# Kernel tuning notes

Measured on AMD Instinct MI355X. Metric: run time of the kernel, lower is better.

Reference implementation:

```python
import jax, jax.numpy as jnp
import numpy as np

NUM_EXPERTS = 16
HIDDEN_DIM = 1024
TOP_K = 4
INPUT_DIM = 4096
OUTPUT_DIM = 4096
BATCH = 4096


def setup_inputs() -> dict:
    key = jax.random.key(0)
    ks = jax.random.split(key, 6)
    total_cols = NUM_EXPERTS * HIDDEN_DIM
    return {
        "x": jax.random.normal(ks[0], (BATCH, INPUT_DIM), dtype=jnp.float32),
        "gate_w": jax.random.normal(ks[1], (INPUT_DIM, NUM_EXPERTS), dtype=jnp.float32) * 0.02,
        "gate_b": jnp.zeros((NUM_EXPERTS,), dtype=jnp.float32),
        "weight": jax.random.normal(ks[2], (INPUT_DIM, total_cols), dtype=jnp.float32) * 0.01,
        "agg_w": jax.random.normal(ks[3], (total_cols, OUTPUT_DIM), dtype=jnp.float32) * 0.02,
        "agg_b": jnp.zeros((OUTPUT_DIM,), dtype=jnp.float32),
    }


def reference(x, gate_w, gate_b, weight, agg_w, agg_b):
    # 1) gating logits (batch, E), 2) sum over batch -> (E,)
    gating_logits = x @ gate_w + gate_b
    gating_sum = gating_logits.sum(axis=0)
    # 3) global top-k expert selection -> binary mask over experts
    _, topk_inds = jax.lax.top_k(gating_sum, TOP_K)
    expert_mask = jnp.zeros((NUM_EXPERTS,), dtype=x.dtype).at[topk_inds].set(1.0)
    # 4/5) block-sparse matmul: mask replicated over all row blocks, so each
    # expert's column block [e*H:(e+1)*H] is x @ W_block if selected else 0.
    out_sparse = x @ weight  # (batch, E*H)
    col_mask = jnp.repeat(expert_mask, HIDDEN_DIM)  # (E*H,)
    out_sparse = out_sparse * col_mask[None, :]
    # 6) aggregator
    final_out = out_sparse @ agg_w + agg_b
    return final_out
```

## Files before the change

kernel.cpp:

```cpp
#include <hip/hip_runtime.h>
#include <hip/hip_bf16.h>


#define BATCH 4096
#define DIN 4096
#define NE 16
#define HD 1024
#define TOPK 4
#define TOTC (NE * HD)
#define NT 64

using bf16 = __hip_bfloat16;
typedef __attribute__((ext_vector_type(8))) short short8;
typedef __attribute__((ext_vector_type(4))) float f32x4;

__device__ inline short f2bs(float f) {
  __hip_bfloat16 h = __float2bfloat16(f);
  return *reinterpret_cast<short*>(&h);
}

__global__ void k_cvtsum(const float* __restrict__ x, bf16* __restrict__ xb,
                         float* __restrict__ colsum) {
  const int t = threadIdx.x;
  const int lane = t & 63;
  const int w = t >> 6;
  const int c = blockIdx.x * 256 + lane * 4;
  const int r0 = blockIdx.y * 128 + w * 32;
  float4 s = {0.f, 0.f, 0.f, 0.f};
  for (int i = 0; i < 32; ++i) {
    size_t off = (size_t)(r0 + i) * DIN + c;
    float4 v = *reinterpret_cast<const float4*>(x + off);
    s.x += v.x; s.y += v.y; s.z += v.z; s.w += v.w;
    ushort4 b;
    b.x = (unsigned short)f2bs(v.x); b.y = (unsigned short)f2bs(v.y);
    b.z = (unsigned short)f2bs(v.z); b.w = (unsigned short)f2bs(v.w);
    *reinterpret_cast<ushort4*>(reinterpret_cast<char*>(xb) + off * 2) = b;
  }
  __shared__ float sm[4][256];
  sm[w][lane * 4 + 0] = s.x; sm[w][lane * 4 + 1] = s.y;
  sm[w][lane * 4 + 2] = s.z; sm[w][lane * 4 + 3] = s.w;
  __syncthreads();
  float tot = sm[0][t] + sm[1][t] + sm[2][t] + sm[3][t];
  atomicAdd(&colsum[blockIdx.x * 256 + t], tot);
}

__global__ void k_gate(const float* __restrict__ colsum, const float* __restrict__ gw,
                       const float* __restrict__ gb, int* __restrict__ ids) {
  __shared__ float red[4][16];
  __shared__ float gs[16];
  int t = threadIdx.x;
  int e = t & 15, kg = t >> 4;
  float p = 0.f;
  for (int k = kg; k < DIN; k += 16) p += colsum[k] * gw[(size_t)k * NE + e];
  p += __shfl_down(p, 32);
  p += __shfl_down(p, 16);
  if ((t & 63) < 16) red[t >> 6][e] = p;
  __syncthreads();
  if (t < 16) gs[t] = red[0][t] + red[1][t] + red[2][t] + red[3][t] + (float)BATCH * gb[t];
  __syncthreads();
  if (t == 0) {
    float v[16];
    #pragma unroll
    for (int i = 0; i < 16; ++i) v[i] = gs[i];
    for (int j = 0; j < TOPK; ++j) {
      int bi = 0;
      float bv = v[0];
      for (int i2 = 1; i2 < 16; ++i2)
        if (v[i2] > bv) { bv = v[i2]; bi = i2; }
      ids[j] = bi;
      v[bi] = -3.4e38f;
    }
  }
}

__global__ void k_gather_w(const float* __restrict__ w, const int* __restrict__ ids,
                           bf16* __restrict__ wbt) {
  __shared__ float tile[64 * 65];
  const int t = threadIdx.x;
  const int tc = t & 15, kr = t >> 4;
  const int tk = t & 7, nr = t >> 3;
  for (int tl = blockIdx.x; tl < 4096; tl += 1024) {
    const int k0 = (tl & 63) * 64, n0 = (tl >> 6) * 64;
    const int e = ids[n0 >> 10];
    const int wc0 = e * HD + (n0 & 1023);
    #pragma unroll
    for (int j = 0; j < 2; ++j) {
      int kk = kr + j * 32;
      float4 v = *reinterpret_cast<const float4*>(w + (size_t)(k0 + kk) * TOTC + wc0 + tc * 4);
      float* dst = &tile[kk * 65 + tc * 4];
      dst[0] = v.x; dst[1] = v.y; dst[2] = v.z; dst[3] = v.w;
    }
    __syncthreads();
    short8 r;
    #pragma unroll
    for (int m = 0; m < 8; ++m) r[m] = f2bs(tile[(tk * 8 + m) * 65 + nr]);
    *reinterpret_cast<short8*>(wbt + (size_t)(n0 + nr) * DIN + k0 + tk * 8) = r;
    __syncthreads();
  }
}

__global__ void k_gather_a(const float* __restrict__ a, const int* __restrict__ ids,
                           bf16* __restrict__ abt) {
  __shared__ float tile[64 * 65];
  const int t = threadIdx.x;
  const int tc = t & 15, kr = t >> 4;
  const int tk = t & 7, nr = t >> 3;
  for (int tl = blockIdx.x; tl < 4096; tl += 1024) {
    const int k0 = (tl & 63) * 64, n0 = (tl >> 6) * 64;
    const int e = ids[k0 >> 10];
    const int ar0 = e * HD + (k0 & 1023);
    #pragma unroll
    for (int j = 0; j < 2; ++j) {
      int kk = kr + j * 32;
      float4 v = *reinterpret_cast<const float4*>(a + (size_t)(ar0 + kk) * 4096 + n0 + tc * 4);
      float* dst = &tile[kk * 65 + tc * 4];
      dst[0] = v.x; dst[1] = v.y; dst[2] = v.z; dst[3] = v.w;
    }
    __syncthreads();
    short8 r;
    #pragma unroll
    for (int m = 0; m < 8; ++m) r[m] = f2bs(tile[(tk * 8 + m) * 65 + nr]);
    *reinterpret_cast<short8*>(abt + (size_t)(n0 + nr) * DIN + k0 + tk * 8) = r;
    __syncthreads();
  }
}

#define MFMA_BF16 __builtin_amdgcn_mfma_f32_16x16x32_bf16
#define VM4 asm volatile("s_waitcnt vmcnt(4)" ::: "memory")
#define VM0 asm volatile("s_waitcnt vmcnt(0)" ::: "memory")
#define NOST ((void)0)

#define PH(BUF, Q, STG, GATE)                                                   \
  do {                                                                          \
    if ((Q) == 0) {                                                             \
      _Pragma("unroll") for (int nf = 0; nf < 4; ++nf) {                        \
        bfrag[nf][0] = LDB(BUF, nf, 0);                                         \
        bfrag[nf][1] = LDB(BUF, nf, 1);                                         \
      }                                                                         \
    }                                                                           \
    short8 aA0 = LDA(BUF, 2 * (Q), 0), aA1 = LDA(BUF, 2 * (Q), 1);              \
    short8 aB0 = LDA(BUF, 2 * (Q) + 1, 0), aB1 = LDA(BUF, 2 * (Q) + 1, 1);      \
    STG;                                                                        \
    GATE;                                                                       \
    __builtin_amdgcn_sched_barrier(0);                                          \
    __builtin_amdgcn_s_barrier();                                               \
    asm volatile("s_waitcnt lgkmcnt(0)" ::: "memory");                          \
    __builtin_amdgcn_sched_barrier(0);                                          \
    __builtin_amdgcn_s_setprio(1);                                              \
    _Pragma("unroll") for (int nf = 0; nf < 4; ++nf) {                          \
      acc[2 * (Q)][nf] = MFMA_BF16(aA0, bfrag[nf][0], acc[2 * (Q)][nf], 0, 0, 0);       \
      acc[2 * (Q)][nf] = MFMA_BF16(aA1, bfrag[nf][1], acc[2 * (Q)][nf], 0, 0, 0);       \
      acc[2 * (Q) + 1][nf] = MFMA_BF16(aB0, bfrag[nf][0], acc[2 * (Q) + 1][nf], 0, 0, 0); \
      acc[2 * (Q) + 1][nf] = MFMA_BF16(aB1, bfrag[nf][1], acc[2 * (Q) + 1][nf], 0, 0, 0); \
    }                                                                           \
    __builtin_amdgcn_s_setprio(0);                                              \
    __builtin_amdgcn_s_barrier();                                               \
  } while (0)

template <int STORE_F32>
__global__ __launch_bounds__(512, 2) void k_gemm8(
    const bf16* __restrict__ A, const bf16* __restrict__ Bt,
    bf16* __restrict__ Cb, float* __restrict__ Cf, const float* __restrict__ bias) {
  __shared__ __align__(16) char smraw[131072];
  const int t = threadIdx.x;
  const int lane = t & 63;
  const int w = t >> 6;
  const int wr = w >> 2;
  const int wc = w & 3;

  const int bid = blockIdx.x;
  const int xcd = bid & 7;
  const int i = bid >> 3;
  const int bm = ((xcd >> 1) * 4 + (i & 3)) * 256;
  const int bn = ((xcd & 1) * 8 + (i >> 2)) * 256;

  f32x4 acc[8][4] = {};
  short8 bfrag[4][2];

  const int srow = w * 16 + (lane >> 3);
  const int sgr = lane & 7;

  auto STAGE_A = [&](int buf, int half, int kt) {
    char* lb = smraw + buf * 65536 + half * 16384 + w * 2048 + lane * 16;
    #pragma unroll
    for (int i2 = 0; i2 < 2; ++i2) {
      int r = srow + i2 * 8;
      const bf16* g = A + (size_t)(bm + half * 128 + r) * 4096 + kt * 64 + ((sgr ^ (r & 7)) * 8);
      __builtin_amdgcn_global_load_lds(
          (const __attribute__((address_space(1))) void*)g,
          (__attribute__((address_space(3))) void*)(lb + i2 * 1024), 16, 0, 0);
    }
  };
  auto STAGE_B = [&](int buf, int half, int kt) {
    char* lb = smraw + buf * 65536 + 32768 + half * 16384 + w * 2048 + lane * 16;
    #pragma unroll
    for (int i2 = 0; i2 < 2; ++i2) {
      int r = srow + i2 * 8;
      const bf16* g = Bt + (size_t)(bn + half * 128 + r) * 4096 + kt * 64 + ((sgr ^ (r & 7)) * 8);
      __builtin_amdgcn_global_load_lds(
          (const __attribute__((address_space(1))) void*)g,
          (__attribute__((address_space(3))) void*)(lb + i2 * 1024), 16, 0, 0);
    }
  };
  auto LDA = [&](int buf, int mf, int kk) -> short8 {
    int r = mf * 16 + (lane & 15);
    int kb = ((kk * 4 + (lane >> 4)) ^ (r & 7)) * 16;
    return *reinterpret_cast<const short8*>(smraw + buf * 65536 + wr * 16384 + r * 128 + kb);
  };
  auto LDB = [&](int buf, int nf, int kk) -> short8 {
    int nc = wc * 64 + nf * 16 + (lane & 15);
    int half = nc >> 7, r = nc & 127;
    int kb = ((kk * 4 + (lane >> 4)) ^ (r & 7)) * 16;
    return *reinterpret_cast<const short8*>(smraw + buf * 65536 + 32768 + half * 16384 + r * 128 + kb);
  };

  STAGE_B(0, 0, 0); STAGE_B(0, 1, 0);
  STAGE_A(0, 0, 0); STAGE_A(0, 1, 0);
  STAGE_B(1, 0, 1); STAGE_B(1, 1, 1);
  VM4;
  __builtin_amdgcn_s_barrier();

  for (int tt = 0; tt < 31; ++tt) {
    const int a = 2 * tt;
    PH(0, 0, STAGE_A(1, 0, a + 1), NOST);
    PH(0, 1, STAGE_A(1, 1, a + 1), NOST);
    PH(0, 2, STAGE_B(0, 0, a + 2), NOST);
    PH(0, 3, STAGE_B(0, 1, a + 2), VM4);
    PH(1, 0, STAGE_A(0, 0, a + 2), NOST);
    PH(1, 1, STAGE_A(0, 1, a + 2), NOST);
    PH(1, 2, STAGE_B(1, 0, a + 3), NOST);
    PH(1, 3, STAGE_B(1, 1, a + 3), VM4);
  }
  PH(0, 0, STAGE_A(1, 0, 63), NOST);
  PH(0, 1, STAGE_A(1, 1, 63), NOST);
  PH(0, 2, NOST, NOST);
  PH(0, 3, NOST, VM0);
  PH(1, 0, NOST, NOST);
  PH(1, 1, NOST, NOST);
  PH(1, 2, NOST, NOST);
  PH(1, 3, NOST, NOST);

  const int cr = (lane >> 4) * 4;
  const int cc = lane & 15;
  #pragma unroll
  for (int mf = 0; mf < 8; ++mf) {
    #pragma unroll
    for (int nf = 0; nf < 4; ++nf) {
      int row = bm + wr * 128 + mf * 16 + cr;
      int col = bn + wc * 64 + nf * 16 + cc;
      #pragma unroll
      for (int r = 0; r < 4; ++r) {
        if constexpr (STORE_F32) {
          Cf[(size_t)(row + r) * 4096 + col] = acc[mf][nf][r] + bias[col];
        } else {
          Cb[(size_t)(row + r) * 4096 + col] = __float2bfloat16(acc[mf][nf][r]);
        }
      }
    }
  }
}

extern "C" void kernel_launch(void* const* d_in, const int* in_sizes, int n_in,
                              void* d_out, int out_size, void* d_ws, size_t ws_size,
                              hipStream_t stream) {
  const float* x = (const float*)d_in[0];
  const float* gate_w = (const float*)d_in[1];
  const float* gate_b = (const float*)d_in[2];
  const float* weight = (const float*)d_in[3];
  const float* agg_w = (const float*)d_in[4];
  const float* agg_b = (const float*)d_in[5];
  float* out = (float*)d_out;
  char* ws = (char*)d_ws;

  float* colsum = (float*)ws;
  int* ids = (int*)(ws + 16384);
  bf16* mid = (bf16*)(ws + (4u << 20));
  bf16* abt = (bf16*)(ws + (36u << 20));
  bf16* xb = (bf16*)d_out;
  bf16* wbt = (bf16*)((char*)d_out + (32u << 20));

  hipMemsetAsync(colsum, 0, DIN * sizeof(float), stream);
  k_cvtsum<<<dim3(16, 32), 256, 0, stream>>>(x, xb, colsum);
  k_gate<<<1, 256, 0, stream>>>(colsum, gate_w, gate_b, ids);
  k_gather_w<<<1024, 512, 0, stream>>>(weight, ids, wbt);
  k_gemm8<0><<<256, 512, 0, stream>>>(xb, wbt, mid, nullptr, nullptr);
  k_gather_a<<<1024, 512, 0, stream>>>(agg_w, ids, abt);
  k_gemm8<1><<<256, 512, 0, stream>>>(mid, abt, nullptr, out, agg_b);
}
```

Measured before the change: 389.5 us.

## Merge weight gathers into one kernel and double-buffer B fragments in GEMM

Fuses the two gather/transpose/convert kernels for the expert weight and aggregator weight into a single launch of 2048 blocks of 256 threads, with each thread now loading four rows. This removes one launch and lets both gathers run concurrently. In the GEMM, the B-fragment LDS reads move out of the first phase of each buffer into a prefetch issued in the previous buffer's last phase, using two register sets (even and odd). The intent is to hide LDS latency behind MFMAs, at the cost of higher VGPR pressure under launch_bounds(512,2).

```diff
diff --git a/kernel.cpp b/kernel.cpp
--- a/kernel.cpp
+++ b/kernel.cpp
@@ -73,54 +73,48 @@
   }
 }
 
-__global__ void k_gather_w(const float* __restrict__ w, const int* __restrict__ ids,
-                           bf16* __restrict__ wbt) {
+__global__ void k_gather(const float* __restrict__ w, const float* __restrict__ a,
+                         const int* __restrict__ ids,
+                         bf16* __restrict__ wbt, bf16* __restrict__ abt) {
   __shared__ float tile[64 * 65];
   const int t = threadIdx.x;
   const int tc = t & 15, kr = t >> 4;
-  const int tk = t & 7, nr = t >> 3;
-  for (int tl = blockIdx.x; tl < 4096; tl += 1024) {
-    const int k0 = (tl & 63) * 64, n0 = (tl >> 6) * 64;
-    const int e = ids[n0 >> 10];
-    const int wc0 = e * HD + (n0 & 1023);
-    #pragma unroll
-    for (int j = 0; j < 2; ++j) {
-      int kk = kr + j * 32;
-      float4 v = *reinterpret_cast<const float4*>(w + (size_t)(k0 + kk) * TOTC + wc0 + tc * 4);
-      float* dst = &tile[kk * 65 + tc * 4];
-      dst[0] = v.x; dst[1] = v.y; dst[2] = v.z; dst[3] = v.w;
+  const int tk = t & 7, nr0 = t >> 3;
+  for (int tl = blockIdx.x; tl < 8192; tl += 2048) {
+    const int wsel = tl < 4096;
+    const int tidx = wsel ? tl : tl - 4096;
+    const int k0 = (tidx & 63) * 64, n0 = (tidx >> 6) * 64;
+    if (wsel) {
+      const int e = ids[n0 >> 10];
+      const int wc0 = e * HD + (n0 & 1023);
+      #pragma unroll
+      for (int j = 0; j < 4; ++j) {
+        int kk = kr + j * 16;
+        float4 v = *reinterpret_cast<const float4*>(w + (size_t)(k0 + kk) * TOTC + wc0 + tc * 4);
+        float* dst = &tile[kk * 65 + tc * 4];
+        dst[0] = v.x; dst[1] = v.y; dst[2] = v.z; dst[3] = v.w;
+      }
+    } else {
+      const int e = ids[k0 >> 10];
+      const int ar0 = e * HD + (k0 & 1023);
+      #pragma unroll
+      for (int j = 0; j < 4; ++j) {
+        int kk = kr + j * 16;
+        float4 v = *reinterpret_cast<const float4*>(a + (size_t)(ar0 + kk) * 4096 + n0 + tc * 4);
+        float* dst = &tile[kk * 65 + tc * 4];
+        dst[0] = v.x; dst[1] = v.y; dst[2] = v.z; dst[3] = v.w;
+      }
     }
     __syncthreads();
-    short8 r;
-    #pragma unroll
-    for (int m = 0; m < 8; ++m) r[m] = f2bs(tile[(tk * 8 + m) * 65 + nr]);
-    *reinterpret_cast<short8*>(wbt + (size_t)(n0 + nr) * DIN + k0 + tk * 8) = r;
-    __syncthreads();
-  }
-}
-
-__global__ void k_gather_a(const float* __restrict__ a, const int* __restrict__ ids,
-                           bf16* __restrict__ abt) {
-  __shared__ float tile[64 * 65];
-  const int t = threadIdx.x;
-  const int tc = t & 15, kr = t >> 4;
-  const int tk = t & 7, nr = t >> 3;
-  for (int tl = blockIdx.x; tl < 4096; tl += 1024) {
-    const int k0 = (tl & 63) * 64, n0 = (tl >> 6) * 64;
-    const int e = ids[k0 >> 10];
-    const int ar0 = e * HD + (k0 & 1023);
-    #pragma unroll
-    for (int j = 0; j < 2; ++j) {
-      int kk = kr + j * 32;
-      float4 v = *reinterpret_cast<const float4*>(a + (size_t)(ar0 + kk) * 4096 + n0 + tc * 4);
-      float* dst = &tile[kk * 65 + tc * 4];
-      dst[0] = v.x; dst[1] = v.y; dst[2] = v.z; dst[3] = v.w;
-    }
-    __syncthreads();
-    short8 r;
-    #pragma unroll
-    for (int m = 0; m < 8; ++m) r[m] = f2bs(tile[(tk * 8 + m) * 65 + nr]);
-    *reinterpret_cast<short8*>(abt + (size_t)(n0 + nr) * DIN + k0 + tk * 8) = r;
+    bf16* dstp = wsel ? wbt : abt;
+    #pragma unroll
+    for (int i = 0; i < 2; ++i) {
+      int n = n0 + nr0 + i * 32;
+      short8 r;
+      #pragma unroll
+      for (int m = 0; m < 8; ++m) r[m] = f2bs(tile[(tk * 8 + m) * 65 + nr0 + i * 32]);
+      *reinterpret_cast<short8*>(dstp + (size_t)n * DIN + k0 + tk * 8) = r;
+    }
     __syncthreads();
   }
 }
@@ -129,15 +123,10 @@
 #define VM4 asm volatile("s_waitcnt vmcnt(4)" ::: "memory")
 #define VM0 asm volatile("s_waitcnt vmcnt(0)" ::: "memory")
 #define NOST ((void)0)
-
-#define PH(BUF, Q, STG, GATE)                                                   \
+#define NOPREF ((void)0)
+
+#define PH(BUF, Q, BF, STG, GATE, PREF)                                         \
   do {                                                                          \
-    if ((Q) == 0) {                                                             \
-      _Pragma("unroll") for (int nf = 0; nf < 4; ++nf) {                        \
-        bfrag[nf][0] = LDB(BUF, nf, 0);                                         \
-        bfrag[nf][1] = LDB(BUF, nf, 1);                                         \
-      }                                                                         \
-    }                                                                           \
     short8 aA0 = LDA(BUF, 2 * (Q), 0), aA1 = LDA(BUF, 2 * (Q), 1);              \
     short8 aB0 = LDA(BUF, 2 * (Q) + 1, 0), aB1 = LDA(BUF, 2 * (Q) + 1, 1);      \
     STG;                                                                        \
@@ -146,16 +135,23 @@
     __builtin_amdgcn_s_barrier();                                               \
     asm volatile("s_waitcnt lgkmcnt(0)" ::: "memory");                          \
     __builtin_amdgcn_sched_barrier(0);                                          \
+    PREF;                                                                       \
     __builtin_amdgcn_s_setprio(1);                                              \
     _Pragma("unroll") for (int nf = 0; nf < 4; ++nf) {                          \
-      acc[2 * (Q)][nf] = MFMA_BF16(aA0, bfrag[nf][0], acc[2 * (Q)][nf], 0, 0, 0);       \
-      acc[2 * (Q)][nf] = MFMA_BF16(aA1, bfrag[nf][1], acc[2 * (Q)][nf], 0, 0, 0);       \
-      acc[2 * (Q) + 1][nf] = MFMA_BF16(aB0, bfrag[nf][0], acc[2 * (Q) + 1][nf], 0, 0, 0); \
-      acc[2 * (Q) + 1][nf] = MFMA_BF16(aB1, bfrag[nf][1], acc[2 * (Q) + 1][nf], 0, 0, 0); \
+      acc[2 * (Q)][nf] = MFMA_BF16(aA0, BF[nf][0], acc[2 * (Q)][nf], 0, 0, 0);          \
+      acc[2 * (Q)][nf] = MFMA_BF16(aA1, BF[nf][1], acc[2 * (Q)][nf], 0, 0, 0);          \
+      acc[2 * (Q) + 1][nf] = MFMA_BF16(aB0, BF[nf][0], acc[2 * (Q) + 1][nf], 0, 0, 0);  \
+      acc[2 * (Q) + 1][nf] = MFMA_BF16(aB1, BF[nf][1], acc[2 * (Q) + 1][nf], 0, 0, 0);  \
     }                                                                           \
     __builtin_amdgcn_s_setprio(0);                                              \
     __builtin_amdgcn_s_barrier();                                               \
   } while (0)
+
+#define PREF_INTO(BF, BUF)                                                      \
+  _Pragma("unroll") for (int nf = 0; nf < 4; ++nf) {                            \
+    BF[nf][0] = LDB(BUF, nf, 0);                                                \
+    BF[nf][1] = LDB(BUF, nf, 1);                                                \
+  }
 
 template <int STORE_F32>
 __global__ __launch_bounds__(512, 2) void k_gemm8(
@@ -175,7 +171,8 @@
   const int bn = ((xcd & 1) * 8 + (i >> 2)) * 256;
 
   f32x4 acc[8][4] = {};
-  short8 bfrag[4][2];
+  short8 bfragE[4][2];
+  short8 bfragO[4][2];
 
   const int srow = w * 16 + (lane >> 3);
   const int sgr = lane & 7;
@@ -219,26 +216,27 @@
   STAGE_B(1, 0, 1); STAGE_B(1, 1, 1);
   VM4;
   __builtin_amdgcn_s_barrier();
+  PREF_INTO(bfragE, 0)
 
   for (int tt = 0; tt < 31; ++tt) {
     const int a = 2 * tt;
-    PH(0, 0, STAGE_A(1, 0, a + 1), NOST);
-    PH(0, 1, STAGE_A(1, 1, a + 1), NOST);
-    PH(0, 2, STAGE_B(0, 0, a + 2), NOST);
-    PH(0, 3, STAGE_B(0, 1, a + 2), VM4);
-    PH(1, 0, STAGE_A(0, 0, a + 2), NOST);
-    PH(1, 1, STAGE_A(0, 1, a + 2), NOST);
-    PH(1, 2, STAGE_B(1, 0, a + 3), NOST);
-    PH(1, 3, STAGE_B(1, 1, a + 3), VM4);
-  }
-  PH(0, 0, STAGE_A(1, 0, 63), NOST);
-  PH(0, 1, STAGE_A(1, 1, 63), NOST);
-  PH(0, 2, NOST, NOST);
-  PH(0, 3, NOST, VM0);
-  PH(1, 0, NOST, NOST);
-  PH(1, 1, NOST, NOST);
-  PH(1, 2, NOST, NOST);
-  PH(1, 3, NOST, NOST);
+    PH(0, 0, bfragE, STAGE_A(1, 0, a + 1), NOST, NOPREF);
+    PH(0, 1, bfragE, STAGE_A(1, 1, a + 1), NOST, NOPREF);
+    PH(0, 2, bfragE, STAGE_B(0, 0, a + 2), NOST, NOPREF);
+    PH(0, 3, bfragE, STAGE_B(0, 1, a + 2), VM4, PREF_INTO(bfragO, 1));
+    PH(1, 0, bfragO, STAGE_A(0, 0, a + 2), NOST, NOPREF);
+    PH(1, 1, bfragO, STAGE_A(0, 1, a + 2), NOST, NOPREF);
+    PH(1, 2, bfragO, STAGE_B(1, 0, a + 3), NOST, NOPREF);
+    PH(1, 3, bfragO, STAGE_B(1, 1, a + 3), VM4, PREF_INTO(bfragE, 0));
+  }
+  PH(0, 0, bfragE, STAGE_A(1, 0, 63), NOST, NOPREF);
+  PH(0, 1, bfragE, STAGE_A(1, 1, 63), NOST, NOPREF);
+  PH(0, 2, bfragE, NOST, NOST, NOPREF);
+  PH(0, 3, bfragE, NOST, VM0, PREF_INTO(bfragO, 1));
+  PH(1, 0, bfragO, NOST, NOST, NOPREF);
+  PH(1, 1, bfragO, NOST, NOST, NOPREF);
+  PH(1, 2, bfragO, NOST, NOST, NOPREF);
+  PH(1, 3, bfragO, NOST, NOST, NOPREF);
 
   const int cr = (lane >> 4) * 4;
   const int cc = lane & 15;
@@ -282,8 +280,7 @@
   hipMemsetAsync(colsum, 0, DIN * sizeof(float), stream);
   k_cvtsum<<<dim3(16, 32), 256, 0, stream>>>(x, xb, colsum);
   k_gate<<<1, 256, 0, stream>>>(colsum, gate_w, gate_b, ids);
-  k_gather_w<<<1024, 512, 0, stream>>>(weight, ids, wbt);
+  k_gather<<<2048, 256, 0, stream>>>(weight, agg_w, ids, wbt, abt);
   k_gemm8<0><<<256, 512, 0, stream>>>(xb, wbt, mid, nullptr, nullptr);
-  k_gather_a<<<1024, 512, 0, stream>>>(agg_w, ids, abt);
   k_gemm8<1><<<256, 512, 0, stream>>>(mid, abt, nullptr, out, agg_b);
 }
```

Result: no change. 387.1 us (-0.6%).
